# Optimization experiments

Measured on AMD Instinct MI355X. Metric: run time of the kernel, lower is better.

Reference implementation:

```python
import jax, jax.numpy as jnp
import numpy as np

N_NODES = 50000
N_EDGES = 800000
F_IN = 128
HIDDEN = 256
N_CLASSES = 4


def setup_inputs() -> dict:
    key = jax.random.key(0)
    k1, k2, k3, k4 = jax.random.split(key, 4)
    x = jax.random.normal(k1, (N_NODES, F_IN), dtype=jnp.float32)
    edge_index = jax.random.randint(k2, (2, N_EDGES), 0, N_NODES, dtype=jnp.int64)
    # Glorot-style init for the two GCNConv linear layers (PyG GCNConv: W then bias)
    s1 = (6.0 / (F_IN + HIDDEN)) ** 0.5
    s2 = (6.0 / (HIDDEN + N_CLASSES)) ** 0.5
    W1 = jax.random.uniform(k3, (F_IN, HIDDEN), jnp.float32, -s1, s1)
    W2 = jax.random.uniform(k4, (HIDDEN, N_CLASSES), jnp.float32, -s2, s2)
    b1 = jnp.zeros((HIDDEN,), jnp.float32)
    b2 = jnp.zeros((N_CLASSES,), jnp.float32)
    return {"x": x, "edge_index": edge_index, "W1": W1, "b1": b1, "W2": W2, "b2": b2}


def _gcn_conv(x, W, b, src, dst, n_nodes):
    # PyG GCNConv: h = x @ W; add self-loops; symmetric D^{-1/2}(A+I)D^{-1/2} aggregation; + bias
    h = x @ W                                            # [N, out]
    deg = jnp.zeros((n_nodes,), h.dtype).at[dst].add(1.0) + 1.0  # +1 for self-loop
    dis = jax.lax.rsqrt(deg)                             # deg^{-1/2}
    norm = dis[src] * dis[dst]                           # [E]
    msg = norm[:, None] * h[src]                         # [E, out] per-edge messages
    agg = jax.ops.segment_sum(msg, dst, num_segments=n_nodes)
    agg = agg + (dis * dis)[:, None] * h                 # self-loop contribution
    return agg + b


def reference(x, edge_index, W1, b1, W2, b2):
    src, dst = edge_index[0], edge_index[1]
    h = _gcn_conv(x, W1, b1, src, dst, N_NODES)
    h = jax.nn.relu(h)
    # F.dropout with training=False (eval/inference reference) is identity
    out = _gcn_conv(h, W2, b2, src, dst, N_NODES)
    return out
```

## Files before the change

kernel.cpp:

```cpp
#include <hip/hip_runtime.h>

#define F_IN   128
#define HIDDEN 256
#define NCLS   4

#define BSH    7
#define BNODES 128
#define BCAP   3072
#define CHUNK  4096
#define NCAP   64

typedef __attribute__((ext_vector_type(8))) short short8;
typedef __attribute__((ext_vector_type(4))) float f32x4;

__device__ __forceinline__ unsigned short f2bf(float f) {
    unsigned int u = __float_as_uint(f);
    return (unsigned short)((u + 0x7fffu + ((u >> 16) & 1u)) >> 16);
}

__device__ __forceinline__ float bflo(unsigned int u) { return __uint_as_float(u << 16); }
__device__ __forceinline__ float bfhi(unsigned int u) { return __uint_as_float(u & 0xffff0000u); }


__global__ __launch_bounds__(256) void k_bin(const int* __restrict__ srcIdx,
                                             const int* __restrict__ dstIdx,
                                             int* __restrict__ cursor,
                                             unsigned int* __restrict__ inter,
                                             int E, int nbuk) {
    __shared__ int cntS[512], bA[512], bB[512], curS[512], eS[512], gS[512];
    __shared__ unsigned int stag[CHUNK];
    __shared__ unsigned short bb[CHUNK];
    int t = threadIdx.x;
    int e0 = blockIdx.x * CHUNK;
    int n = E - e0; if (n > CHUNK) n = CHUNK;

    cntS[t] = 0; cntS[t + 256] = 0;
    __syncthreads();
    for (int i = t; i < n; i += 256)
        atomicAdd(&cntS[dstIdx[e0 + i] >> BSH], 1);
    __syncthreads();

    int* pa = bA; int* pb = bB;
    bA[t] = cntS[t]; bA[t + 256] = cntS[t + 256];
    __syncthreads();
    for (int off = 1; off < 512; off <<= 1) {
        pb[t] = pa[t] + (t >= off ? pa[t - off] : 0);
        int p1 = t + 256;
        pb[p1] = pa[p1] + (p1 >= off ? pa[p1 - off] : 0);
        __syncthreads();
        int* tmp = pa; pa = pb; pb = tmp;
    }
    eS[t] = pa[t] - cntS[t];
    curS[t] = eS[t];
    int p1 = t + 256;
    eS[p1] = pa[p1] - cntS[p1];
    curS[p1] = eS[p1];
    __syncthreads();

    for (int i = t; i < nbuk; i += 256) {
        int c = cntS[i];
        gS[i] = (c > 0) ? atomicAdd(&cursor[i], c) : 0;
    }
    __syncthreads();

    for (int i = t; i < n; i += 256) {
        int d = dstIdx[e0 + i];
        int s = srcIdx[e0 + i];
        int b = d >> BSH;
        unsigned int w = ((unsigned int)(d & (BNODES - 1)) << 16) | (unsigned int)s;
        int off = atomicAdd(&curS[b], 1);
        stag[off] = w;
        bb[off] = (unsigned short)b;
    }
    __syncthreads();

    for (int i = t; i < n; i += 256) {
        int b = bb[i];
        inter[(size_t)b * BCAP + gS[b] + (i - eS[b])] = stag[i];
    }
}


__global__ __launch_bounds__(256) void k_bucket_build(const unsigned int* __restrict__ inter,
                                                      const int* __restrict__ cursor,
                                                      const float2* __restrict__ x2,
                                                      float* __restrict__ dis,
                                                      int* __restrict__ degPad,
                                                      unsigned int* __restrict__ xs,
                                                      unsigned short* __restrict__ csr16,
                                                      int N, int nbuk) {
    __shared__ int cntS[BNODES], curS[BNODES];
    __shared__ float disS[BNODES];
    int t = threadIdx.x;
    int b = blockIdx.x;
    int node0 = b << BSH;
    int nloc = N - node0; if (nloc > BNODES) nloc = BNODES;
    int cntb = cursor[b];
    const unsigned int* ip = inter + (size_t)b * BCAP;

    if (t < BNODES) { cntS[t] = 0; curS[t] = 0; }
    __syncthreads();
    for (int i = t; i < cntb; i += 256)
        atomicAdd(&cntS[ip[i] >> 16], 1);
    __syncthreads();

    if (t < nloc) {
        int c = cntS[t];
        float d = rsqrtf((float)c + 1.0f);
        dis[node0 + t] = d;
        disS[t] = d;
        degPad[node0 + t] = (c + 7) & ~7;
    }
    __syncthreads();

    for (int i = t; i < cntb; i += 256) {
        unsigned int w = ip[i];
        int nl = w >> 16;
        int off = atomicAdd(&curS[nl], 1);
        csr16[((size_t)(node0 + nl)) * NCAP + off] = (unsigned short)(w & 0xffffu);
    }
    if (t < nloc) {
        int c = cntS[t], p = (c + 7) & ~7;
        for (int k = c; k < p; ++k)
            csr16[((size_t)(node0 + t)) * NCAP + k] = (unsigned short)N;
    }

    for (int i = t; i < nloc * 64; i += 256) {
        int nl = i >> 6, l = i & 63;
        float d = disS[nl];
        float2 v = x2[((size_t)(node0 + nl)) * 64 + l];
        xs[((size_t)(node0 + nl)) * 64 + l] =
            (unsigned int)f2bf(d * v.x) | ((unsigned int)f2bf(d * v.y) << 16);
    }
    if (b == 0) {
        if (t < 64) xs[(size_t)N * 64 + t] = 0u;
        if (t == 64) dis[N] = 0.f;
    }
}


__global__ __launch_bounds__(256) void k_sort(unsigned short* __restrict__ csr16,
                                              const int* __restrict__ degPad, int N) {
    int wave = threadIdx.x >> 6;
    int node = blockIdx.x * 4 + wave;
    int l = threadIdx.x & 63;
    if (node >= N) return;
    int dp = degPad[node];
    unsigned short* cp = csr16 + (size_t)node * NCAP;
    int v = (l < dp) ? (int)cp[l] : 0xFFFF;
#pragma unroll
    for (int k = 2; k <= 64; k <<= 1) {
#pragma unroll
        for (int j = k >> 1; j > 0; j >>= 1) {
            int p = __shfl_xor(v, j);
            int mn = p < v ? p : v;
            int mx = p < v ? v : p;
            bool up = ((l & k) == 0);
            bool lower = ((l & j) == 0);
            v = (up == lower) ? mn : mx;
        }
    }
    if (l < dp) cp[l] = (unsigned short)v;
}


__global__ __launch_bounds__(256) void k_w1f_zero(const float* __restrict__ W1,
                                                  unsigned short* __restrict__ W1f,
                                                  int* __restrict__ cursor, int nbuk) {
    int t = blockIdx.x * 256 + threadIdx.x;
    if (t < nbuk) cursor[t] = 0;
    int lane = t & 63;
    int ks = (t >> 6) & 3;
    int ct = t >> 8;
    int n = ct * 16 + (lane & 15);
    int k0 = ks * 32 + (lane >> 4) * 8;
    unsigned int w[4];
#pragma unroll
    for (int p = 0; p < 4; ++p) {
        unsigned int lo = f2bf(W1[(k0 + 2 * p + 0) * HIDDEN + n]);
        unsigned int hi = f2bf(W1[(k0 + 2 * p + 1) * HIDDEN + n]);
        w[p] = lo | (hi << 16);
    }
    *(uint4*)(W1f + (size_t)t * 8) = make_uint4(w[0], w[1], w[2], w[3]);
}


__global__ __launch_bounds__(256) void k_pull_x(const unsigned short* __restrict__ csr16,
                                                const int* __restrict__ degPad,
                                                const float* __restrict__ dis,
                                                const unsigned int* __restrict__ xs,
                                                const float2* __restrict__ x2,
                                                unsigned int* __restrict__ aggB, int N) {
    int wave = threadIdx.x >> 6;
    int node = blockIdx.x * 4 + wave;
    int l = threadIdx.x & 63;
    if (node >= N) return;
    int dp = degPad[node];
    const unsigned short* cp = csr16 + (size_t)node * NCAP;
    float ax = 0.f, ay = 0.f;
    for (int e = 0; e < dp; e += 8) {
        uint4 iv = *(const uint4*)(cp + e);
        int s0 = iv.x & 0xffff, s1 = iv.x >> 16;
        int s2 = iv.y & 0xffff, s3 = iv.y >> 16;
        int s4 = iv.z & 0xffff, s5 = iv.z >> 16;
        int s6 = iv.w & 0xffff, s7 = iv.w >> 16;
        unsigned int u0 = xs[(size_t)s0 * 64 + l];
        unsigned int u1 = xs[(size_t)s1 * 64 + l];
        unsigned int u2 = xs[(size_t)s2 * 64 + l];
        unsigned int u3 = xs[(size_t)s3 * 64 + l];
        unsigned int u4 = xs[(size_t)s4 * 64 + l];
        unsigned int u5 = xs[(size_t)s5 * 64 + l];
        unsigned int u6 = xs[(size_t)s6 * 64 + l];
        unsigned int u7 = xs[(size_t)s7 * 64 + l];
        ax += bflo(u0) + bflo(u1) + bflo(u2) + bflo(u3) + bflo(u4) + bflo(u5) + bflo(u6) + bflo(u7);
        ay += bfhi(u0) + bfhi(u1) + bfhi(u2) + bfhi(u3) + bfhi(u4) + bfhi(u5) + bfhi(u6) + bfhi(u7);
    }
    float dd = dis[node];
    float sd = dd * dd;
    float2 xv = x2[(size_t)node * 64 + l];
    float ox = dd * ax + sd * xv.x;
    float oy = dd * ay + sd * xv.y;
    aggB[(size_t)node * 64 + l] = (unsigned int)f2bf(ox) | ((unsigned int)f2bf(oy) << 16);
}


__global__ __launch_bounds__(256) void k_gemm_mfma(const unsigned short* __restrict__ aggB,
                                                   const unsigned short* __restrict__ W1f,
                                                   const float* __restrict__ b1,
                                                   const float* __restrict__ W2,
                                                   float* __restrict__ Z, int N) {
    int wave = threadIdx.x >> 6;
    int lane = threadIdx.x & 63;
    int tile = blockIdx.x * 4 + wave;
    int row0 = tile * 16;
    if (row0 > N) return;
    int q = lane >> 4;
    int c16 = lane & 15;

    short8 a[4];
    const unsigned short* arow = aggB + (size_t)(row0 + c16) * F_IN;
#pragma unroll
    for (int ks = 0; ks < 4; ++ks)
        a[ks] = *(const short8*)(arow + ks * 32 + q * 8);

    float p[4][4] = {{0.f}};
#pragma unroll
    for (int ct = 0; ct < 16; ++ct) {
        f32x4 c = {0.f, 0.f, 0.f, 0.f};
#pragma unroll
        for (int ks = 0; ks < 4; ++ks) {
            short8 b = *(const short8*)(W1f + ((size_t)((ct * 4 + ks) * 64 + lane)) * 8);
            c = __builtin_amdgcn_mfma_f32_16x16x32_bf16(a[ks], b, c, 0, 0, 0);
        }
        int n = ct * 16 + c16;
        float bias = b1[n];
        float4 w2v = *(const float4*)(W2 + n * NCLS);
#pragma unroll
        for (int r = 0; r < 4; ++r) {
            float h = c[r] + bias;
            h = h > 0.f ? h : 0.f;
            p[r][0] += h * w2v.x;
            p[r][1] += h * w2v.y;
            p[r][2] += h * w2v.z;
            p[r][3] += h * w2v.w;
        }
    }
#pragma unroll
    for (int m = 1; m < 16; m <<= 1) {
#pragma unroll
        for (int r = 0; r < 4; ++r) {
#pragma unroll
            for (int j = 0; j < 4; ++j)
                p[r][j] += __shfl_xor(p[r][j], m);
        }
    }
    if (c16 == 0) {
#pragma unroll
        for (int r = 0; r < 4; ++r) {
            int row = row0 + q * 4 + r;
            if (row < N)
                *(float4*)(Z + (size_t)row * NCLS) = make_float4(p[r][0], p[r][1], p[r][2], p[r][3]);
            else if (row == N)
                *(float4*)(Z + (size_t)row * NCLS) = make_float4(0.f, 0.f, 0.f, 0.f);
        }
    }
}


__global__ __launch_bounds__(256) void k_pull_z(const unsigned short* __restrict__ csr16,
                                                const int* __restrict__ degPad,
                                                const float* __restrict__ dis,
                                                const float* __restrict__ Z,
                                                const float* __restrict__ b2,
                                                float* __restrict__ out, int N) {
    int t = blockIdx.x * blockDim.x + threadIdx.x;
    int node = t >> 2;
    int j = t & 3;
    if (node >= N) return;
    int dp = degPad[node];
    const unsigned short* cp = csr16 + (size_t)node * NCAP;
    float acc = 0.f;
    for (int e = 0; e < dp; e += 8) {
        uint4 iv = *(const uint4*)(cp + e);
        int s0 = iv.x & 0xffff, s1 = iv.x >> 16;
        int s2 = iv.y & 0xffff, s3 = iv.y >> 16;
        int s4 = iv.z & 0xffff, s5 = iv.z >> 16;
        int s6 = iv.w & 0xffff, s7 = iv.w >> 16;
        acc += dis[s0] * Z[(size_t)s0 * NCLS + j] + dis[s1] * Z[(size_t)s1 * NCLS + j]
             + dis[s2] * Z[(size_t)s2 * NCLS + j] + dis[s3] * Z[(size_t)s3 * NCLS + j]
             + dis[s4] * Z[(size_t)s4 * NCLS + j] + dis[s5] * Z[(size_t)s5 * NCLS + j]
             + dis[s6] * Z[(size_t)s6 * NCLS + j] + dis[s7] * Z[(size_t)s7 * NCLS + j];
    }
    float dd = dis[node];
    out[(size_t)node * NCLS + j] = dd * acc + dd * dd * Z[(size_t)node * NCLS + j] + b2[j];
}


extern "C" void kernel_launch(void* const* d_in, const int* in_sizes, int n_in,
                              void* d_out, int out_size, void* d_ws, size_t ws_size,
                              hipStream_t stream) {
    const float* x      = (const float*)d_in[0];
    const int*   ei     = (const int*)d_in[1];
    const float* W1     = (const float*)d_in[2];
    const float* b1     = (const float*)d_in[3];
    const float* W2     = (const float*)d_in[4];
    const float* b2     = (const float*)d_in[5];
    float* out          = (float*)d_out;

    const int N = in_sizes[0] / F_IN;
    const int E = in_sizes[1] / 2;
    const int* srcIdx = ei;
    const int* dstIdx = ei + E;

    const int nbuk = (N + BNODES - 1) >> BSH;

    unsigned short* aggB = (unsigned short*)d_ws;
    unsigned short* xsB  = aggB + (size_t)(N + 16) * F_IN;
    unsigned short* W1f  = xsB + (size_t)(N + 8) * F_IN;
    float* Z    = (float*)(W1f + 32768);
    float* dis  = Z + (size_t)(N + 4) * NCLS;
    int* degPad = (int*)(dis + N + 4);
    int* cursor = degPad + N;
    unsigned short* csr16 = (unsigned short*)(cursor + 512);
    unsigned int* inter = (unsigned int*)(csr16 + (size_t)N * NCAP);

    k_w1f_zero<<<16, 256, 0, stream>>>(W1, W1f, cursor, nbuk);
    k_bin<<<(E + CHUNK - 1) / CHUNK, 256, 0, stream>>>(srcIdx, dstIdx, cursor, inter, E, nbuk);
    k_bucket_build<<<nbuk, 256, 0, stream>>>(inter, cursor, (const float2*)x,
                                             dis, degPad, (unsigned int*)xsB, csr16, N, nbuk);
    k_sort<<<(N + 3) / 4, 256, 0, stream>>>(csr16, degPad, N);
    k_pull_x<<<(N + 3) / 4, 256, 0, stream>>>(csr16, degPad, dis, (const unsigned int*)xsB,
                                              (const float2*)x, (unsigned int*)aggB, N);
    const int nTiles = N / 16 + 1;
    k_gemm_mfma<<<(nTiles + 3) / 4, 256, 0, stream>>>(aggB, W1f, b1, W2, Z, N);
    k_pull_z<<<(N * 4 + 255) / 256, 256, 0, stream>>>(csr16, degPad, dis, Z, b2, out, N);
}
```

Baseline: 180.8 us.

## Fold self-loop into CSR lists and fuse neighbor sort into bucket build

Each node's self-loop is now added as an explicit entry in its padded CSR neighbor list. This removes the separate self-loop terms (the extra x read in pull_x and the Z/dis reads in pull_z). The per-node bitonic sort moves from its own kernel into the end of k_bucket_build, with each wave sorting up to 32 nodes of its bucket, which saves one launch and a reread of degPad. In exchange, self-loops now go through bf16-scaled xs instead of fp32 x, which slightly changes precision. Padding also grows by one slot for nodes whose degree is a multiple of 8, and sorting now runs with fewer waves in flight.

After: 203.1 us. 12.3% more time.

```diff
diff --git a/kernel.cpp b/kernel.cpp
--- a/kernel.cpp
+++ b/kernel.cpp
@@ -109,7 +109,7 @@
         float d = rsqrtf((float)c + 1.0f);
         dis[node0 + t] = d;
         disS[t] = d;
-        degPad[node0 + t] = (c + 7) & ~7;
+        degPad[node0 + t] = (c + 8) & ~7;
     }
     __syncthreads();
 
@@ -120,9 +120,10 @@
         csr16[((size_t)(node0 + nl)) * NCAP + off] = (unsigned short)(w & 0xffffu);
     }
     if (t < nloc) {
-        int c = cntS[t], p = (c + 7) & ~7;
-        for (int k = c; k < p; ++k)
-            csr16[((size_t)(node0 + t)) * NCAP + k] = (unsigned short)N;
+        int c = cntS[t], p = (c + 8) & ~7;
+        unsigned short* cp = csr16 + ((size_t)(node0 + t)) * NCAP;
+        cp[c] = (unsigned short)(node0 + t);
+        for (int k = c + 1; k < p; ++k) cp[k] = (unsigned short)N;
     }
 
     for (int i = t; i < nloc * 64; i += 256) {
@@ -136,31 +137,29 @@
         if (t < 64) xs[(size_t)N * 64 + t] = 0u;
         if (t == 64) dis[N] = 0.f;
     }
-}
-
-
-__global__ __launch_bounds__(256) void k_sort(unsigned short* __restrict__ csr16,
-                                              const int* __restrict__ degPad, int N) {
-    int wave = threadIdx.x >> 6;
-    int node = blockIdx.x * 4 + wave;
-    int l = threadIdx.x & 63;
-    if (node >= N) return;
-    int dp = degPad[node];
-    unsigned short* cp = csr16 + (size_t)node * NCAP;
-    int v = (l < dp) ? (int)cp[l] : 0xFFFF;
-#pragma unroll
-    for (int k = 2; k <= 64; k <<= 1) {
-#pragma unroll
-        for (int j = k >> 1; j > 0; j >>= 1) {
-            int p = __shfl_xor(v, j);
-            int mn = p < v ? p : v;
-            int mx = p < v ? v : p;
-            bool up = ((l & k) == 0);
-            bool lower = ((l & j) == 0);
-            v = (up == lower) ? mn : mx;
-        }
-    }
-    if (l < dp) cp[l] = (unsigned short)v;
+    __syncthreads();
+
+    int wave = t >> 6, l = t & 63;
+    for (int i = 0; i < 32; ++i) {
+        int widx = wave * 32 + i;
+        if (widx >= nloc) break;
+        int dp = (cntS[widx] + 8) & ~7;
+        unsigned short* cp = csr16 + ((size_t)(node0 + widx)) * NCAP;
+        int v = (l < dp) ? (int)cp[l] : 0xFFFF;
+#pragma unroll
+        for (int k = 2; k <= 64; k <<= 1) {
+#pragma unroll
+            for (int j = k >> 1; j > 0; j >>= 1) {
+                int p = __shfl_xor(v, j);
+                int mn = p < v ? p : v;
+                int mx = p < v ? v : p;
+                bool up = ((l & k) == 0);
+                bool lower = ((l & j) == 0);
+                v = (up == lower) ? mn : mx;
+            }
+        }
+        if (l < dp) cp[l] = (unsigned short)v;
+    }
 }
 
 
@@ -189,7 +188,6 @@
                                                 const int* __restrict__ degPad,
                                                 const float* __restrict__ dis,
                                                 const unsigned int* __restrict__ xs,
-                                                const float2* __restrict__ x2,
                                                 unsigned int* __restrict__ aggB, int N) {
     int wave = threadIdx.x >> 6;
     int node = blockIdx.x * 4 + wave;
@@ -216,11 +214,7 @@
         ay += bfhi(u0) + bfhi(u1) + bfhi(u2) + bfhi(u3) + bfhi(u4) + bfhi(u5) + bfhi(u6) + bfhi(u7);
     }
     float dd = dis[node];
-    float sd = dd * dd;
-    float2 xv = x2[(size_t)node * 64 + l];
-    float ox = dd * ax + sd * xv.x;
-    float oy = dd * ay + sd * xv.y;
-    aggB[(size_t)node * 64 + l] = (unsigned int)f2bf(ox) | ((unsigned int)f2bf(oy) << 16);
+    aggB[(size_t)node * 64 + l] = (unsigned int)f2bf(dd * ax) | ((unsigned int)f2bf(dd * ay) << 16);
 }
 
 
@@ -311,8 +305,7 @@
              + dis[s4] * Z[(size_t)s4 * NCLS + j] + dis[s5] * Z[(size_t)s5 * NCLS + j]
              + dis[s6] * Z[(size_t)s6 * NCLS + j] + dis[s7] * Z[(size_t)s7 * NCLS + j];
     }
-    float dd = dis[node];
-    out[(size_t)node * NCLS + j] = dd * acc + dd * dd * Z[(size_t)node * NCLS + j] + b2[j];
+    out[(size_t)node * NCLS + j] = dis[node] * acc + b2[j];
 }
 
 
@@ -348,9 +341,8 @@
     k_bin<<<(E + CHUNK - 1) / CHUNK, 256, 0, stream>>>(srcIdx, dstIdx, cursor, inter, E, nbuk);
     k_bucket_build<<<nbuk, 256, 0, stream>>>(inter, cursor, (const float2*)x,
                                              dis, degPad, (unsigned int*)xsB, csr16, N, nbuk);
-    k_sort<<<(N + 3) / 4, 256, 0, stream>>>(csr16, degPad, N);
     k_pull_x<<<(N + 3) / 4, 256, 0, stream>>>(csr16, degPad, dis, (const unsigned int*)xsB,
-                                              (const float2*)x, (unsigned int*)aggB, N);
+                                              (unsigned int*)aggB, N);
     const int nTiles = N / 16 + 1;
     k_gemm_mfma<<<(nTiles + 3) / 4, 256, 0, stream>>>(aggB, W1f, b1, W2, Z, N);
     k_pull_z<<<(N * 4 + 255) / 256, 256, 0, stream>>>(csr16, degPad, dis, Z, b2, out, N);
```
